# Performance work log

Measured on AMD Instinct MI355X. Metric: run time of the kernel, lower is better.

Reference implementation:

```python
import math
import jax, jax.numpy as jnp
import numpy as np

B, C_IN, H, W = 16, 384, 64, 64
CDIM, K, NSCALES, ITERS = 128, 64, 2, 3

def conv1x1(x, w, b):
    # x: [B,C,H,W], w: [O,C], b: [O]
    return jnp.einsum('bchw,oc->bohw', x, w) + b[None, :, None, None]

def mlp2(x, w1, b1, w2, b2):
    return conv1x1(jax.nn.relu(conv1x1(x, w1, b1)), w2, b2)

def log_optimal_transport(scores, dustbin, iters):
    B_, K_, N_ = scores.shape
    Z = jnp.concatenate([scores, dustbin], axis=1)  # [B,K+1,N]
    log_mu = jnp.full((B_, K_ + 1), -math.log(K_ + 1), dtype=scores.dtype)
    log_nu = jnp.full((B_, N_), -math.log(N_), dtype=scores.dtype)
    u = jnp.zeros_like(log_mu)
    v = jnp.zeros_like(log_nu)
    for _ in range(iters):
        u = log_mu - jax.nn.logsumexp(Z + v[:, None, :], axis=2)
        v = log_nu - jax.nn.logsumexp(Z + u[:, :, None], axis=1)
    return Z + u[:, :, None] + v[:, None, :]

def avg_pool2(x):
    b, c, h, w = x.shape
    return x.reshape(b, c, h // 2, 2, w // 2, 2).mean(axis=(3, 5))

def scale_branch(xs, fw1, fb1, fw2, fb2, sw1, sb1, sw2, sb2, dw1, db1, dw2, db2):
    b = xs.shape[0]
    local_feat = mlp2(xs, fw1, fb1, fw2, fb2).reshape(b, CDIM, -1)   # [B,C,N]
    score = mlp2(xs, sw1, sb1, sw2, sb2).reshape(b, K, -1)           # [B,K,N]
    dustbin = mlp2(xs, dw1, db1, dw2, db2).reshape(b, 1, -1)         # [B,1,N]
    log_p = log_optimal_transport(score, dustbin, ITERS)
    p = jnp.exp(log_p)[:, :-1, :]                                    # drop dustbin row
    p = p / (p.sum(axis=-1, keepdims=True) + 1e-8)
    out = jnp.einsum('bcn,bkn->bck', local_feat, p)                  # [B,C,K]
    out = out / jnp.clip(jnp.linalg.norm(out, axis=1, keepdims=True), 1e-12)
    return out.reshape(b, -1), local_feat

def setup_inputs():
    key = jax.random.key(0)
    ks = jax.random.split(key, 13)
    inp = {'x': jax.random.normal(ks[0], (B, C_IN, H, W), jnp.float32)}
    kidx = 1
    for s in range(NSCALES):
        for name, (o, i) in [('fw1', (512, C_IN)), ('fw2', (CDIM, 512)),
                              ('sw1', (512, C_IN)), ('sw2', (K, 512)),
                              ('dw1', (128, C_IN)), ('dw2', (1, 128))]:
            inp[f'{name}_{s}'] = 0.02 * jax.random.normal(ks[kidx % 13], (o, i), jnp.float32)
            inp[f'{name[0]}b{name[2]}_{s}'] = jnp.zeros((o,), jnp.float32)
            kidx += 1
    return inp

def reference(x,
              fw1_0, fb1_0, fw2_0, fb2_0, sw1_0, sb1_0, sw2_0, sb2_0, dw1_0, db1_0, dw2_0, db2_0,
              fw1_1, fb1_1, fw2_1, fb2_1, sw1_1, sb1_1, sw2_1, sb2_1, dw1_1, db1_1, dw2_1, db2_1):
    params = [
        (fw1_0, fb1_0, fw2_0, fb2_0, sw1_0, sb1_0, sw2_0, sb2_0, dw1_0, db1_0, dw2_0, db2_0),
        (fw1_1, fb1_1, fw2_1, fb2_1, sw1_1, sb1_1, sw2_1, sb2_1, dw1_1, db1_1, dw2_1, db2_1),
    ]
    descs = []
    xs = x
    for s in range(NSCALES):
        if s > 0:
            xs = avg_pool2(xs)
        d, _ = scale_branch(xs, *params[s])
        descs.append(d)
    g = jnp.stack(descs, axis=1).mean(axis=1)
    g = g / jnp.clip(jnp.linalg.norm(g, axis=1, keepdims=True), 1e-12)
    return g
```

## Files before the change

kernel.cpp:

```cpp
#include <hip/hip_runtime.h>
#include <math.h>

typedef __attribute__((ext_vector_type(8))) short short8;
typedef __attribute__((ext_vector_type(4))) float floatx4;

__device__ inline float bf2f(short s) {
    union { unsigned u; float f; } x; x.u = ((unsigned)(unsigned short)s) << 16; return x.f;
}
__device__ inline short f2bf(float f) {
    union { float f; unsigned u; } x; x.f = f;
    unsigned r = x.u + 0x7fff + ((x.u >> 16) & 1);
    return (short)(r >> 16);
}

struct WSet {
    const float *fw1, *fb1, *fw2, *sw1, *sb1, *sw2, *sb2, *dw1, *db1, *dw2, *db2;
};

__device__ inline void wprep_core(const WSet A,
    short* __restrict__ W1f, short* __restrict__ W2af, short* __restrict__ W2bf,
    float* __restrict__ B1p, float* __restrict__ B2bp, int id)
{
    if (id < 491520) {
        int e = id & 7, l = (id >> 3) & 63, g = (id >> 9) & 15, rest = id >> 13;
        int kc = rest % 12, c = rest / 12;
        int m = c * 256 + g * 16 + (l & 15);
        int k = kc * 32 + (l >> 4) * 8 + e;
        float v = 0.f;
        if (m < 512) v = A.fw1[m * 384 + k];
        else if (m < 1024) v = A.sw1[(m - 512) * 384 + k];
        else if (m < 1152) v = A.dw1[(m - 1024) * 384 + k];
        W1f[id] = f2bf(v);
        return;
    }
    id -= 491520;
    if (id < 65536) {
        int e = id & 7, l = (id >> 3) & 63, g = (id >> 9) & 7, ka = id >> 12;
        int r = g * 16 + (l & 15), k = ka * 32 + (l >> 4) * 8 + e;
        W2af[id] = f2bf(A.fw2[r * 512 + k]);
        return;
    }
    id -= 65536;
    if (id < 98304) {
        int e = id & 7, l = (id >> 3) & 63, g = (id >> 9) & 7, kb = id >> 12;
        int r = g * 16 + (l & 15), krel = kb * 32 + (l >> 4) * 8 + e;
        float v = 0.f;
        if (r < 64 && krel < 512) v = A.sw2[r * 512 + krel];
        else if (r == 64 && krel >= 512 && krel < 640) v = A.dw2[krel - 512];
        W2bf[id] = f2bf(v);
        return;
    }
    id -= 98304;
    if (id < 1280) {
        float v = 0.f;
        if (id < 512) v = A.fb1[id];
        else if (id < 1024) v = A.sb1[id - 512];
        else if (id < 1152) v = A.db1[id - 1024];
        B1p[id] = v;
        return;
    }
    id -= 1280;
    if (id < 128) B2bp[id] = id < 64 ? A.sb2[id] : id == 64 ? A.db2[0] : 0.f;
}

__device__ inline void xprep_core(const float* __restrict__ x,
                                  short* __restrict__ xT, short* __restrict__ x1T,
                                  float* xt, int ip, int cg, int b, int t)
{
    #pragma unroll
    for (int u = 0; u < 8; u++) {
        int idx = t + 256 * u;
        int c = idx >> 5, spq = idx & 31;
        float4 v = *(const float4*)&x[(((long)b * 384 + cg * 64 + c) * 64 + ip * 2 + (spq >> 4)) * 64 + (spq & 15) * 4];
        float* d = &xt[c * 129 + spq * 4];
        d[0] = v.x; d[1] = v.y; d[2] = v.z; d[3] = v.w;
    }
    __syncthreads();
    {
        int sp = t >> 1, ch = t & 1;
        short tmp[32];
        #pragma unroll
        for (int cc = 0; cc < 32; cc++) tmp[cc] = f2bf(xt[(ch * 32 + cc) * 129 + sp]);
        short* dst = xT + ((long)b * 4096 + ip * 128 + sp) * 384 + cg * 64 + ch * 32;
        #pragma unroll
        for (int v = 0; v < 4; v++) *(short8*)(dst + v * 8) = *(short8*)(tmp + v * 8);
    }
    {
        int j1 = t >> 3, c8 = t & 7;
        short tmp[8];
        #pragma unroll
        for (int e = 0; e < 8; e++) {
            int c = c8 * 8 + e;
            float v = 0.25f * (xt[c * 129 + j1 * 2]      + xt[c * 129 + j1 * 2 + 1] +
                               xt[c * 129 + 64 + j1 * 2] + xt[c * 129 + 64 + j1 * 2 + 1]);
            tmp[e] = f2bf(v);
        }
        *(short8*)(x1T + ((long)b * 1024 + ip * 32 + j1) * 384 + cg * 64 + c8 * 8) = *(short8*)tmp;
    }
}

__global__ __launch_bounds__(256) void wprep(WSet a0, WSet a1,
    short* __restrict__ W1f, short* __restrict__ W2af, short* __restrict__ W2bf,
    float* __restrict__ B1p, float* __restrict__ B2bp)
{
    const int s = blockIdx.y;
    const WSet A = s ? a1 : a0;
    wprep_core(A, W1f + (size_t)s * 491520, W2af + (size_t)s * 65536,
               W2bf + (size_t)s * 98304, B1p + s * 1280, B2bp + s * 128,
               blockIdx.x * 256 + threadIdx.x);
}

__global__ __launch_bounds__(256) void xprep(const float* __restrict__ x,
                                             short* __restrict__ xT, short* __restrict__ x1T)
{
    __shared__ float xt[64 * 129];
    xprep_core(x, xT, x1T, xt, blockIdx.x, blockIdx.y, blockIdx.z, threadIdx.x);
}

__global__ __launch_bounds__(256) void prep(WSet a0, WSet a1,
    short* __restrict__ W1f, short* __restrict__ W2af, short* __restrict__ W2bf,
    float* __restrict__ B1p, float* __restrict__ B2bp,
    const float* __restrict__ x, short* __restrict__ xT, short* __restrict__ x1T)
{
    __shared__ float xt[64 * 129];
    const int bid = blockIdx.x, t = threadIdx.x;
    if (bid < 5132) {
        const int s = bid >= 2566;
        const WSet A = s ? a1 : a0;
        wprep_core(A, W1f + (size_t)s * 491520, W2af + (size_t)s * 65536,
                   W2bf + (size_t)s * 98304, B1p + s * 1280, B2bp + s * 128,
                   (bid - (s ? 2566 : 0)) * 256 + t);
    } else {
        const int xb = bid - 5132;
        xprep_core(x, xT, x1T, xt, xb & 31, (xb >> 5) % 6, (xb >> 5) / 6, t);
    }
}

__global__ __launch_bounds__(512, 4) void fused_mlp(
    const short* __restrict__ W1f_, const float* __restrict__ B1p_,
    const short* __restrict__ W2af_, const float* __restrict__ fb2_0, const float* __restrict__ fb2_1,
    const short* __restrict__ W2bf_, const float* __restrict__ B2bp_,
    const short* __restrict__ xT, const short* __restrict__ x1T,
    float* __restrict__ feat0, float* __restrict__ feat1,
    short* __restrict__ Eg0, short* __restrict__ Eg1,
    float* __restrict__ pu0, float* __restrict__ pu1)
{
    __shared__ short xs[12 * 2048];
    __shared__ short hs[8 * 2048];
    const int tid = threadIdx.x;
    const int wid = tid >> 6, lane = tid & 63;
    const int l15 = lane & 15, q = lane >> 4;
    const int bx = blockIdx.x, b = blockIdx.y;
    const int sc = bx >= 64;
    const int tile = sc ? bx - 64 : bx;
    const int N = sc ? 1024 : 4096;
    const int n0 = tile * 64;
    const short* XT = sc ? x1T : xT;
    const short* W1f = W1f_ + (size_t)sc * 491520;
    const float* B1p = B1p_ + sc * 1280;
    const short* W2af = W2af_ + (size_t)sc * 65536;
    const short* W2bf = W2bf_ + (size_t)sc * 98304;
    const float* fb2 = sc ? fb2_1 : fb2_0;
    const float* B2bp = B2bp_ + sc * 128;
    float* feat = (sc ? feat1 : feat0) + (long)b * 128 * N;
    short* Eg = (sc ? Eg1 : Eg0) + (long)b * 65 * N;
    float* pu = sc ? pu1 : pu0;
    const int npart = sc ? 16 : 64;

    {
        const int n = tid >> 3;
        const int c0 = (tid & 7) * 6;
        const short* src = XT + ((long)b * N + n0 + n) * 384 + c0 * 8;
        const int jj = n >> 4, nl = n & 15;
        #pragma unroll
        for (int i = 0; i < 6; i++) {
            int c = c0 + i;
            int kc = c >> 2, qq = c & 3;
            *(short8*)(xs + kc * 2048 + jj * 512 + ((qq << 4) | nl) * 8) =
                *(const short8*)(src + i * 8);
        }
    }
    __syncthreads();

    floatx4 acc2[2][4];
    #pragma unroll
    for (int i = 0; i < 2; i++)
        #pragma unroll
        for (int j = 0; j < 4; j++) acc2[i][j] = floatx4{0.f, 0.f, 0.f, 0.f};

    auto phase2 = [&](int pc) {
        if (pc < 2) {
            const short* WA = W2af + (size_t)pc * 32768;
            short8 hb[2][4], wa[2];
            #pragma unroll
            for (int j = 0; j < 4; j++) hb[0][j] = *(short8*)(hs + j * 512 + lane * 8);
            wa[0] = *(const short8*)(WA + wid * 512 + lane * 8);
            #pragma unroll
            for (int kc2 = 0; kc2 < 8; kc2++) {
                short8 bfr[4];
                #pragma unroll
                for (int j = 0; j < 4; j++) bfr[j] = hb[kc2 & 1][j];
                short8 aF = wa[kc2 & 1];
                if (kc2 + 1 < 8) {
                    #pragma unroll
                    for (int j = 0; j < 4; j++)
                        hb[(kc2 + 1) & 1][j] = *(short8*)(hs + (kc2 + 1) * 2048 + j * 512 + lane * 8);
                    wa[(kc2 + 1) & 1] = *(const short8*)(WA + ((kc2 + 1) * 8 + wid) * 512 + lane * 8);
                }
                #pragma unroll
                for (int j = 0; j < 4; j++)
                    acc2[0][j] = __builtin_amdgcn_mfma_f32_16x16x32_bf16(aF, bfr[j], acc2[0][j], 0, 0, 0);
            }
        } else {
            if (wid >= 5) return;
            const short* WB = W2bf + (size_t)(pc - 2) * 32768;
            short8 hb[2][4], we[2];
            #pragma unroll
            for (int j = 0; j < 4; j++) hb[0][j] = *(short8*)(hs + j * 512 + lane * 8);
            we[0] = *(const short8*)(WB + wid * 512 + lane * 8);
            #pragma unroll
            for (int kc2 = 0; kc2 < 8; kc2++) {
                short8 bfr[4];
                #pragma unroll
                for (int j = 0; j < 4; j++) bfr[j] = hb[kc2 & 1][j];
                short8 aE = we[kc2 & 1];
                if (kc2 + 1 < 8) {
                    #pragma unroll
                    for (int j = 0; j < 4; j++)
                        hb[(kc2 + 1) & 1][j] = *(short8*)(hs + (kc2 + 1) * 2048 + j * 512 + lane * 8);
                    we[(kc2 + 1) & 1] = *(const short8*)(WB + ((kc2 + 1) * 8 + wid) * 512 + lane * 8);
                }
                #pragma unroll
                for (int j = 0; j < 4; j++)
                    acc2[1][j] = __builtin_amdgcn_mfma_f32_16x16x32_bf16(aE, bfr[j], acc2[1][j], 0, 0, 0);
            }
        }
    };

    for (int c = 0; c < 5; c++) {
        if (c > 0) phase2(c - 1);
        floatx4 acc1[2][4];
        #pragma unroll
        for (int i = 0; i < 2; i++)
            #pragma unroll
            for (int j = 0; j < 4; j++) acc1[i][j] = floatx4{0.f, 0.f, 0.f, 0.f};
        const short* Wb = W1f + (long)c * 98304;
        short8 abuf[2][2];
        #pragma unroll
        for (int i = 0; i < 2; i++) {
            abuf[0][i] = *(const short8*)(Wb + (wid * 2 + i) * 512 + lane * 8);
            abuf[1][i] = *(const short8*)(Wb + (16 + wid * 2 + i) * 512 + lane * 8);
        }
        #pragma unroll
        for (int kc = 0; kc < 12; kc++) {
            short8 ac[2], bc[4];
            #pragma unroll
            for (int i = 0; i < 2; i++) ac[i] = abuf[kc & 1][i];
            #pragma unroll
            for (int j = 0; j < 4; j++) bc[j] = *(short8*)(xs + kc * 2048 + j * 512 + lane * 8);
            if (kc + 2 < 12) {
                #pragma unroll
                for (int i = 0; i < 2; i++)
                    abuf[kc & 1][i] = *(const short8*)(Wb + ((kc + 2) * 16 + wid * 2 + i) * 512 + lane * 8);
            }
            #pragma unroll
            for (int i = 0; i < 2; i++)
                #pragma unroll
                for (int j = 0; j < 4; j++)
                    acc1[i][j] = __builtin_amdgcn_mfma_f32_16x16x32_bf16(ac[i], bc[j], acc1[i][j], 0, 0, 0);
        }
        __syncthreads();
        #pragma unroll
        for (int i = 0; i < 2; i++) {
            const int qf = i * 2 + (q >> 1);
            const int e0 = 4 * (q & 1);
            const int mrow = c * 256 + wid * 32 + i * 16 + q * 4;
            float bw[4];
            #pragma unroll
            for (int rr = 0; rr < 4; rr++) bw[rr] = B1p[mrow + rr];
            #pragma unroll
            for (int j = 0; j < 4; j++) {
                short pk[4];
                #pragma unroll
                for (int rr = 0; rr < 4; rr++)
                    pk[rr] = f2bf(fmaxf(acc1[i][j][rr] + bw[rr], 0.f));
                *(unsigned long long*)(hs + wid * 2048 + j * 512 + ((qf << 4) | l15) * 8 + e0) =
                    *(unsigned long long*)pk;
            }
        }
        __syncthreads();
    }
    phase2(4);

    {
        const int row0 = wid * 16 + q * 4;
        #pragma unroll
        for (int rr = 0; rr < 4; rr++) {
            float bv = fb2[row0 + rr];
            #pragma unroll
            for (int j = 0; j < 4; j++)
                feat[(long)(row0 + rr) * N + n0 + 16 * j + l15] = acc2[0][j][rr] + bv;
        }
    }
    __syncthreads();
    float* puld = (float*)hs;
    if (wid < 4) {
        #pragma unroll
        for (int rr = 0; rr < 4; rr++) {
            int row = wid * 16 + q * 4 + rr;
            float bv = B2bp[row];
            float s = 0.f;
            #pragma unroll
            for (int j = 0; j < 4; j++) {
                float e = expf(acc2[1][j][rr] + bv);
                Eg[(long)row * N + n0 + 16 * j + l15] = f2bf(e);
                s += e;
            }
            s += __shfl_xor(s, 1); s += __shfl_xor(s, 2);
            s += __shfl_xor(s, 4); s += __shfl_xor(s, 8);
            if (l15 == 0) puld[row] = s;
        }
    } else if (wid == 4) {
        #pragma unroll
        for (int rr = 0; rr < 4; rr++) {
            int row = 64 + q * 4 + rr;
            bool valid = (row == 64);
            float bv = B2bp[64];
            float s = 0.f;
            #pragma unroll
            for (int j = 0; j < 4; j++) {
                float e = expf(acc2[1][j][rr] + bv);
                if (valid) {
                    Eg[(long)64 * N + n0 + 16 * j + l15] = f2bf(e);
                    s += e;
                }
            }
            s += __shfl_xor(s, 1); s += __shfl_xor(s, 2);
            s += __shfl_xor(s, 4); s += __shfl_xor(s, 8);
            if (valid && l15 == 0) puld[64] = s;
        }
    }
    __syncthreads();
    if (tid < 65)
        pu[((long)b * npart + tile) * 65 + tid] = puld[tid];
}

__global__ __launch_bounds__(256) void sk_step(
    const short* __restrict__ Eg0, const short* __restrict__ Eg1,
    const float* __restrict__ pin0, const float* __restrict__ pin1,
    float* __restrict__ pout0, float* __restrict__ pout1, int nin0, int nin1)
{
    __shared__ short Es[65 * 264];
    __shared__ float evs[256];
    __shared__ float eus[65];
    const int t = threadIdx.x;
    const int bx = blockIdx.x, b = blockIdx.y;
    const int sc = bx >= 16;
    const int chunk = sc ? bx - 16 : bx;
    const int N = sc ? 1024 : 4096;
    const float invN = sc ? (1.0f / 1024.0f) : (1.0f / 4096.0f);
    const int n0 = chunk * 256;
    const short* Eb = (sc ? Eg1 : Eg0) + (long)b * 65 * N;
    const float* pin = sc ? pin1 : pin0;
    const int nin = sc ? nin1 : nin0;
    float* pout = sc ? pout1 : pout0;
    const int nout = sc ? 4 : 16;
    if (t < 65) {
        float s = 0.f;
        for (int ch = 0; ch < nin; ch++) s += pin[((long)b * nin + ch) * 65 + t];
        eus[t] = (1.0f / 65.0f) / s;
    }
    for (int it = t; it < 2080; it += 256) {
        int k = it >> 5, n8 = it & 31;
        *(short8*)(Es + k * 264 + n8 * 8) = *(const short8*)(Eb + (long)k * N + n0 + n8 * 8);
    }
    __syncthreads();
    float sv = 0.f;
    #pragma unroll 4
    for (int k = 0; k < 65; k++) sv += bf2f(Es[k * 264 + t]) * eus[k];
    evs[t] = invN / sv;
    __syncthreads();
    const int wid = t >> 6, lane = t & 63;
    for (int k = wid; k < 65; k += 4) {
        const short* er = Es + k * 264 + lane * 4;
        float4 v4 = *(const float4*)&evs[lane * 4];
        float s = bf2f(er[0]) * v4.x + bf2f(er[1]) * v4.y + bf2f(er[2]) * v4.z + bf2f(er[3]) * v4.w;
        #pragma unroll
        for (int off = 32; off >= 1; off >>= 1) s += __shfl_xor(s, off);
        if (lane == 0) pout[((long)b * nout + chunk) * 65 + k] = s;
    }
}

__global__ __launch_bounds__(256) void sk_desc(
    const short* __restrict__ Eg0, const short* __restrict__ Eg1,
    const float* __restrict__ pin0, const float* __restrict__ pin1,
    const float* __restrict__ feat0, const float* __restrict__ feat1,
    float* __restrict__ part0, float* __restrict__ part1, int nin0, int nin1)
{
    __shared__ short Es[65 * 264];
    __shared__ float eus[65];
    __shared__ float evs[256];
    const int t = threadIdx.x;
    const int bx = blockIdx.x, b = blockIdx.y;
    const int sc = bx >= 16;
    const int chunk = sc ? bx - 16 : bx;
    const int N = sc ? 1024 : 4096;
    const float invN = sc ? (1.0f / 1024.0f) : (1.0f / 4096.0f);
    const int nch = sc ? 4 : 16;
    const int n0 = chunk * 256;
    const short* Eb = (sc ? Eg1 : Eg0) + (long)b * 65 * N;
    const float* pin = sc ? pin1 : pin0;
    const int nin = sc ? nin1 : nin0;
    const float* fb = (sc ? feat1 : feat0) + (long)b * 128 * N;
    float* part = sc ? part1 : part0;
    if (t < 65) {
        float s = 0.f;
        for (int ch = 0; ch < nin; ch++) s += pin[((long)b * nin + ch) * 65 + t];
        eus[t] = (1.0f / 65.0f) / s;
    }
    for (int it = t; it < 2080; it += 256) {
        int k = it >> 5, n8 = it & 31;
        *(short8*)(Es + k * 264 + n8 * 8) = *(const short8*)(Eb + (long)k * N + n0 + n8 * 8);
    }
    __syncthreads();
    float sv = 0.f;
    #pragma unroll 4
    for (int k = 0; k < 65; k++) sv += bf2f(Es[k * 264 + t]) * eus[k];
    evs[t] = invN / sv;
    __syncthreads();
    const int wid = t >> 6, lane = t & 63;
    const int l15 = lane & 15, q = lane >> 4;
    float* pb = part + ((long)b * nch + chunk) * 8256;
    for (int k = wid; k < 64; k += 4) {
        const short* er = Es + k * 264 + lane * 4;
        float4 v4 = *(const float4*)&evs[lane * 4];
        float s = bf2f(er[0]) * v4.x + bf2f(er[1]) * v4.y + bf2f(er[2]) * v4.z + bf2f(er[3]) * v4.w;
        #pragma unroll
        for (int off = 32; off >= 1; off >>= 1) s += __shfl_xor(s, off);
        if (lane == 0) pb[8192 + k] = s * eus[k];
    }
    floatx4 acc[2][4];
    #pragma unroll
    for (int mt = 0; mt < 2; mt++)
        #pragma unroll
        for (int nt = 0; nt < 4; nt++) acc[mt][nt] = floatx4{0.f, 0.f, 0.f, 0.f};
    #pragma unroll 2
    for (int ks = 0; ks < 8; ks++) {
        float4 ev0 = *(const float4*)&evs[ks * 32 + q * 8];
        float4 ev1 = *(const float4*)&evs[ks * 32 + q * 8 + 4];
        float evq[8] = {ev0.x, ev0.y, ev0.z, ev0.w, ev1.x, ev1.y, ev1.z, ev1.w};
        short8 ah[2], al[2];
        #pragma unroll
        for (int mt = 0; mt < 2; mt++) {
            const float* fp = fb + (long)(wid * 32 + mt * 16 + l15) * N + n0 + ks * 32 + q * 8;
            float4 v0 = *(const float4*)fp;
            float4 v1 = *(const float4*)(fp + 4);
            float va[8] = {v0.x, v0.y, v0.z, v0.w, v1.x, v1.y, v1.z, v1.w};
            short hh[8], ll[8];
            #pragma unroll
            for (int e = 0; e < 8; e++) {
                float sv2 = va[e] * evq[e];
                short h = f2bf(sv2);
                hh[e] = h;
                ll[e] = f2bf(sv2 - bf2f(h));
            }
            ah[mt] = *(short8*)hh;
            al[mt] = *(short8*)ll;
        }
        #pragma unroll
        for (int nt = 0; nt < 4; nt++) {
            short8 bfr = *(short8*)(Es + (nt * 16 + l15) * 264 + ks * 32 + q * 8);
            #pragma unroll
            for (int mt = 0; mt < 2; mt++) {
                acc[mt][nt] = __builtin_amdgcn_mfma_f32_16x16x32_bf16(al[mt], bfr, acc[mt][nt], 0, 0, 0);
                acc[mt][nt] = __builtin_amdgcn_mfma_f32_16x16x32_bf16(ah[mt], bfr, acc[mt][nt], 0, 0, 0);
            }
        }
    }
    #pragma unroll
    for (int nt = 0; nt < 4; nt++) {
        float euk = eus[nt * 16 + l15];
        #pragma unroll
        for (int mt = 0; mt < 2; mt++)
            #pragma unroll
            for (int rr = 0; rr < 4; rr++)
                pb[(wid * 32 + mt * 16 + q * 4 + rr) * 64 + nt * 16 + l15] = acc[mt][nt][rr] * euk;
    }
}

__global__ __launch_bounds__(256) void dred_final(
    const float* __restrict__ part0, const float* __restrict__ part1,
    float* __restrict__ out, int b0)
{
    __shared__ float d0s[128 * 65];
    __shared__ float d1s[128 * 65];
    __shared__ float rsv[64];
    __shared__ float red[4];
    const int b = blockIdx.x;
    const int t = threadIdx.x;
    const int c = t >> 1, k0 = (t & 1) * 32;

    #pragma unroll
    for (int s = 0; s < 2; s++) {
        const int nch = s ? 4 : 16;
        const float* pb = (s ? part1 : part0) + (long)b * nch * 8256;
        float* ds = s ? d1s : d0s;
        if (t < 64) {
            float rs = 0.f;
            for (int ch = 0; ch < nch; ch++) rs += pb[ch * 8256 + 8192 + t];
            rsv[t] = 1.0f / (rs + 1e-8f);
        }
        __syncthreads();
        float a[32];
        #pragma unroll 8
        for (int j = 0; j < 32; j++) a[j] = 0.f;
        for (int ch = 0; ch < nch; ch++) {
            const float* p = pb + ch * 8256 + c * 64 + k0;
            #pragma unroll 8
            for (int j = 0; j < 32; j++) a[j] += p[j];
        }
        #pragma unroll 8
        for (int j = 0; j < 32; j++) ds[c * 65 + k0 + j] = a[j] * rsv[k0 + j];
        __syncthreads();
        if (t < 64) {
            float sq = 0.f;
            for (int c2 = 0; c2 < 128; c2++) { float v = ds[c2 * 65 + t]; sq += v * v; }
            rsv[t] = 1.0f / fmaxf(sqrtf(sq), 1e-12f);
        }
        __syncthreads();
        #pragma unroll 8
        for (int j = 0; j < 32; j++) ds[c * 65 + k0 + j] *= rsv[k0 + j];
        __syncthreads();
    }
    float s = 0.f;
    for (int i = t; i < 8192; i += 256) {
        int cc = i >> 6, k = i & 63;
        float v = (d0s[cc * 65 + k] + d1s[cc * 65 + k]) * 0.5f;
        s += v * v;
    }
    const int wave = t >> 6, lane = t & 63;
    #pragma unroll
    for (int off = 32; off >= 1; off >>= 1) s += __shfl_xor(s, off);
    if (lane == 0) red[wave] = s;
    __syncthreads();
    float tot = red[0] + red[1] + red[2] + red[3];
    float inv = 1.0f / fmaxf(sqrtf(tot), 1e-12f);
    float* o = out + (long)(b0 + b) * 8192;
    for (int i = t; i < 8192; i += 256) {
        int cc = i >> 6, k = i & 63;
        o[i] = (d0s[cc * 65 + k] + d1s[cc * 65 + k]) * 0.5f * inv;
    }
}

extern "C" void kernel_launch(void* const* d_in, const int* in_sizes, int n_in,
                              void* d_out, int out_size, void* d_ws, size_t ws_size,
                              hipStream_t stream)
{
    (void)in_sizes; (void)n_in; (void)out_size;
    const float* x = (const float*)d_in[0];
    WSet ws2[2];
    const float* fb2p[2];
    for (int s = 0; s < 2; s++) {
        int o = 1 + s * 12;
        ws2[s].fw1 = (const float*)d_in[o + 0];  ws2[s].fb1 = (const float*)d_in[o + 1];
        ws2[s].fw2 = (const float*)d_in[o + 2];  fb2p[s]    = (const float*)d_in[o + 3];
        ws2[s].sw1 = (const float*)d_in[o + 4];  ws2[s].sb1 = (const float*)d_in[o + 5];
        ws2[s].sw2 = (const float*)d_in[o + 6];  ws2[s].sb2 = (const float*)d_in[o + 7];
        ws2[s].dw1 = (const float*)d_in[o + 8];  ws2[s].db1 = (const float*)d_in[o + 9];
        ws2[s].dw2 = (const float*)d_in[o + 10]; ws2[s].db2 = (const float*)d_in[o + 11];
    }

    const size_t fixed = ((size_t)2*491520*2 + 2*65536*2 + 2*98304*2
                        + 2*1280*4 + 2*128*4) + (1 << 16);
    const size_t perb = (size_t)4096*384*2 + (size_t)1024*384*2
                      + (size_t)128*4096*4 + (size_t)128*1024*4
                      + (size_t)65*4096*2 + (size_t)65*1024*2
                      + (size_t)(64+16)*65*4 + (size_t)(16+4)*65*4
                      + (size_t)16*8256*4 + (size_t)4*8256*4 + 8192;
    int CB = 4;
    const int cand[3] = {16, 8, 4};
    for (int ci = 0; ci < 3; ci++)
        if (fixed + (size_t)cand[ci] * perb <= ws_size) { CB = cand[ci]; break; }

    char* p = (char*)d_ws;
    auto alloc = [&](size_t bytes) -> char* {
        char* r = p; p += (bytes + 255) & ~(size_t)255; return r;
    };
    short* W1f   = (short*)alloc((size_t)2 * 491520 * 2);
    short* W2af  = (short*)alloc((size_t)2 * 65536 * 2);
    short* W2bf  = (short*)alloc((size_t)2 * 98304 * 2);
    float* B1p   = (float*)alloc((size_t)2 * 1280 * 4);
    float* B2bp  = (float*)alloc((size_t)2 * 128 * 4);
    short* xT    = (short*)alloc((size_t)CB * 4096 * 384 * 2);
    short* x1T   = (short*)alloc((size_t)CB * 1024 * 384 * 2);
    float* feat0 = (float*)alloc((size_t)CB * 128 * 4096 * 4);
    float* feat1 = (float*)alloc((size_t)CB * 128 * 1024 * 4);
    short* Eg0   = (short*)alloc((size_t)CB * 65 * 4096 * 2);
    short* Eg1   = (short*)alloc((size_t)CB * 65 * 1024 * 2);
    float* puA0  = (float*)alloc((size_t)CB * 64 * 65 * 4);
    float* puA1  = (float*)alloc((size_t)CB * 16 * 65 * 4);
    float* puB0  = (float*)alloc((size_t)CB * 16 * 65 * 4);
    float* puB1  = (float*)alloc((size_t)CB * 4 * 65 * 4);
    float* part0 = (float*)alloc((size_t)CB * 16 * 8256 * 4);
    float* part1 = (float*)alloc((size_t)CB * 4 * 8256 * 4);

    if (CB == 16) {
        prep<<<dim3(8204), 256, 0, stream>>>(ws2[0], ws2[1],
            W1f, W2af, W2bf, B1p, B2bp, x, xT, x1T);
        fused_mlp<<<dim3(80, 16), 512, 0, stream>>>(
            W1f, B1p, W2af, fb2p[0], fb2p[1], W2bf, B2bp,
            xT, x1T, feat0, feat1, Eg0, Eg1, puA0, puA1);
        sk_step<<<dim3(20, 16), 256, 0, stream>>>(Eg0, Eg1, puA0, puA1, puB0, puB1, 64, 16);
        sk_step<<<dim3(20, 16), 256, 0, stream>>>(Eg0, Eg1, puB0, puB1, puA0, puA1, 16, 4);
        sk_desc<<<dim3(20, 16), 256, 0, stream>>>(Eg0, Eg1, puA0, puA1,
                                                  feat0, feat1, part0, part1, 16, 4);
        dred_final<<<dim3(16), 256, 0, stream>>>(part0, part1, (float*)d_out, 0);
    } else {
        wprep<<<dim3(2566, 2), 256, 0, stream>>>(ws2[0], ws2[1], W1f, W2af, W2bf, B1p, B2bp);
        for (int b0 = 0; b0 < 16; b0 += CB) {
            xprep<<<dim3(32, 6, CB), 256, 0, stream>>>(x + (size_t)b0 * 384 * 4096, xT, x1T);
            fused_mlp<<<dim3(80, CB), 512, 0, stream>>>(
                W1f, B1p, W2af, fb2p[0], fb2p[1], W2bf, B2bp,
                xT, x1T, feat0, feat1, Eg0, Eg1, puA0, puA1);
            sk_step<<<dim3(20, CB), 256, 0, stream>>>(Eg0, Eg1, puA0, puA1, puB0, puB1, 64, 16);
            sk_step<<<dim3(20, CB), 256, 0, stream>>>(Eg0, Eg1, puB0, puB1, puA0, puA1, 16, 4);
            sk_desc<<<dim3(20, CB), 256, 0, stream>>>(Eg0, Eg1, puA0, puA1,
                                                      feat0, feat1, part0, part1, 16, 4);
            dred_final<<<dim3(CB), 256, 0, stream>>>(part0, part1, (float*)d_out, b0);
        }
    }
}
```

Baseline: 410.3 us.

## Split fused prep back into separate kernels and widen final reduction to 1024 threads

```diff
diff --git a/kernel.cpp b/kernel.cpp
--- a/kernel.cpp
+++ b/kernel.cpp
@@ -17,10 +17,18 @@
     const float *fw1, *fb1, *fw2, *sw1, *sb1, *sw2, *sb2, *dw1, *db1, *dw2, *db2;
 };
 
-__device__ inline void wprep_core(const WSet A,
+__global__ __launch_bounds__(256) void wprep(WSet a0, WSet a1,
     short* __restrict__ W1f, short* __restrict__ W2af, short* __restrict__ W2bf,
-    float* __restrict__ B1p, float* __restrict__ B2bp, int id)
+    float* __restrict__ B1p, float* __restrict__ B2bp)
 {
+    const int s = blockIdx.y;
+    const WSet A = s ? a1 : a0;
+    W1f  += (size_t)s * 491520;
+    W2af += (size_t)s * 65536;
+    W2bf += (size_t)s * 98304;
+    B1p  += s * 1280;
+    B2bp += s * 128;
+    int id = blockIdx.x * 256 + threadIdx.x;
     if (id < 491520) {
         int e = id & 7, l = (id >> 3) & 63, g = (id >> 9) & 15, rest = id >> 13;
         int kc = rest % 12, c = rest / 12;
@@ -63,10 +71,14 @@
     if (id < 128) B2bp[id] = id < 64 ? A.sb2[id] : id == 64 ? A.db2[0] : 0.f;
 }
 
-__device__ inline void xprep_core(const float* __restrict__ x,
-                                  short* __restrict__ xT, short* __restrict__ x1T,
-                                  float* xt, int ip, int cg, int b, int t)
+__global__ __launch_bounds__(256) void xprep(const float* __restrict__ x,
+                                             short* __restrict__ xT, short* __restrict__ x1T)
 {
+    __shared__ float xt[64 * 129];
+    const int ip = blockIdx.x;
+    const int cg = blockIdx.y;
+    const int b  = blockIdx.z;
+    const int t  = threadIdx.x;
     #pragma unroll
     for (int u = 0; u < 8; u++) {
         int idx = t + 256 * u;
@@ -96,43 +108,6 @@
             tmp[e] = f2bf(v);
         }
         *(short8*)(x1T + ((long)b * 1024 + ip * 32 + j1) * 384 + cg * 64 + c8 * 8) = *(short8*)tmp;
-    }
-}
-
-__global__ __launch_bounds__(256) void wprep(WSet a0, WSet a1,
-    short* __restrict__ W1f, short* __restrict__ W2af, short* __restrict__ W2bf,
-    float* __restrict__ B1p, float* __restrict__ B2bp)
-{
-    const int s = blockIdx.y;
-    const WSet A = s ? a1 : a0;
-    wprep_core(A, W1f + (size_t)s * 491520, W2af + (size_t)s * 65536,
-               W2bf + (size_t)s * 98304, B1p + s * 1280, B2bp + s * 128,
-               blockIdx.x * 256 + threadIdx.x);
-}
-
-__global__ __launch_bounds__(256) void xprep(const float* __restrict__ x,
-                                             short* __restrict__ xT, short* __restrict__ x1T)
-{
-    __shared__ float xt[64 * 129];
-    xprep_core(x, xT, x1T, xt, blockIdx.x, blockIdx.y, blockIdx.z, threadIdx.x);
-}
-
-__global__ __launch_bounds__(256) void prep(WSet a0, WSet a1,
-    short* __restrict__ W1f, short* __restrict__ W2af, short* __restrict__ W2bf,
-    float* __restrict__ B1p, float* __restrict__ B2bp,
-    const float* __restrict__ x, short* __restrict__ xT, short* __restrict__ x1T)
-{
-    __shared__ float xt[64 * 129];
-    const int bid = blockIdx.x, t = threadIdx.x;
-    if (bid < 5132) {
-        const int s = bid >= 2566;
-        const WSet A = s ? a1 : a0;
-        wprep_core(A, W1f + (size_t)s * 491520, W2af + (size_t)s * 65536,
-                   W2bf + (size_t)s * 98304, B1p + s * 1280, B2bp + s * 128,
-                   (bid - (s ? 2566 : 0)) * 256 + t);
-    } else {
-        const int xb = bid - 5132;
-        xprep_core(x, xT, x1T, xt, xb & 31, (xb >> 5) % 6, (xb >> 5) / 6, t);
     }
 }
 
@@ -488,17 +463,20 @@
     }
 }
 
-__global__ __launch_bounds__(256) void dred_final(
+__global__ __launch_bounds__(1024) void dred_final(
     const float* __restrict__ part0, const float* __restrict__ part1,
     float* __restrict__ out, int b0)
 {
     __shared__ float d0s[128 * 65];
     __shared__ float d1s[128 * 65];
+    __shared__ float colp[16][64];
     __shared__ float rsv[64];
-    __shared__ float red[4];
+    __shared__ float red[16];
     const int b = blockIdx.x;
     const int t = threadIdx.x;
-    const int c = t >> 1, k0 = (t & 1) * 32;
+    const int c = t >> 3;
+    const int k0 = (t & 7) * 8;
+    const int wv = t >> 6, l = t & 63;
 
     #pragma unroll
     for (int s = 0; s < 2; s++) {
@@ -511,45 +489,57 @@
             rsv[t] = 1.0f / (rs + 1e-8f);
         }
         __syncthreads();
-        float a[32];
-        #pragma unroll 8
-        for (int j = 0; j < 32; j++) a[j] = 0.f;
+        float a[8];
+        #pragma unroll
+        for (int j = 0; j < 8; j++) a[j] = 0.f;
         for (int ch = 0; ch < nch; ch++) {
             const float* p = pb + ch * 8256 + c * 64 + k0;
-            #pragma unroll 8
-            for (int j = 0; j < 32; j++) a[j] += p[j];
-        }
-        #pragma unroll 8
-        for (int j = 0; j < 32; j++) ds[c * 65 + k0 + j] = a[j] * rsv[k0 + j];
+            #pragma unroll
+            for (int j = 0; j < 8; j++) a[j] += p[j];
+        }
+        #pragma unroll
+        for (int j = 0; j < 8; j++) a[j] *= rsv[k0 + j];
+        float v[8];
+        #pragma unroll
+        for (int j = 0; j < 8; j++) v[j] = a[j] * a[j];
+        #pragma unroll
+        for (int off = 8; off <= 32; off <<= 1)
+            #pragma unroll
+            for (int j = 0; j < 8; j++) v[j] += __shfl_xor(v[j], off);
+        if (l < 8) {
+            #pragma unroll
+            for (int j = 0; j < 8; j++) colp[wv][l * 8 + j] = v[j];
+        }
         __syncthreads();
         if (t < 64) {
             float sq = 0.f;
-            for (int c2 = 0; c2 < 128; c2++) { float v = ds[c2 * 65 + t]; sq += v * v; }
+            #pragma unroll
+            for (int w2 = 0; w2 < 16; w2++) sq += colp[w2][t];
             rsv[t] = 1.0f / fmaxf(sqrtf(sq), 1e-12f);
         }
         __syncthreads();
-        #pragma unroll 8
-        for (int j = 0; j < 32; j++) ds[c * 65 + k0 + j] *= rsv[k0 + j];
+        #pragma unroll
+        for (int j = 0; j < 8; j++) ds[c * 65 + k0 + j] = a[j] * rsv[k0 + j];
         __syncthreads();
     }
-    float s = 0.f;
-    for (int i = t; i < 8192; i += 256) {
-        int cc = i >> 6, k = i & 63;
-        float v = (d0s[cc * 65 + k] + d1s[cc * 65 + k]) * 0.5f;
-        s += v * v;
-    }
-    const int wave = t >> 6, lane = t & 63;
-    #pragma unroll
-    for (int off = 32; off >= 1; off >>= 1) s += __shfl_xor(s, off);
-    if (lane == 0) red[wave] = s;
-    __syncthreads();
-    float tot = red[0] + red[1] + red[2] + red[3];
+    float g[8];
+    float ssum = 0.f;
+    #pragma unroll
+    for (int j = 0; j < 8; j++) {
+        float v2 = (d0s[c * 65 + k0 + j] + d1s[c * 65 + k0 + j]) * 0.5f;
+        g[j] = v2; ssum += v2 * v2;
+    }
+    #pragma unroll
+    for (int off = 32; off >= 1; off >>= 1) ssum += __shfl_xor(ssum, off);
+    if (l == 0) red[wv] = ssum;
+    __syncthreads();
+    float tot = 0.f;
+    #pragma unroll
+    for (int w2 = 0; w2 < 16; w2++) tot += red[w2];
     float inv = 1.0f / fmaxf(sqrtf(tot), 1e-12f);
-    float* o = out + (long)(b0 + b) * 8192;
-    for (int i = t; i < 8192; i += 256) {
-        int cc = i >> 6, k = i & 63;
-        o[i] = (d0s[cc * 65 + k] + d1s[cc * 65 + k]) * 0.5f * inv;
-    }
+    float* o = out + (long)(b0 + b) * 8192 + c * 64 + k0;
+    #pragma unroll
+    for (int j = 0; j < 8; j++) o[j] = g[j] * inv;
 }
 
 extern "C" void kernel_launch(void* const* d_in, const int* in_sizes, int n_in,
@@ -604,29 +594,16 @@
     float* part0 = (float*)alloc((size_t)CB * 16 * 8256 * 4);
     float* part1 = (float*)alloc((size_t)CB * 4 * 8256 * 4);
 
-    if (CB == 16) {
-        prep<<<dim3(8204), 256, 0, stream>>>(ws2[0], ws2[1],
-            W1f, W2af, W2bf, B1p, B2bp, x, xT, x1T);
-        fused_mlp<<<dim3(80, 16), 512, 0, stream>>>(
+    wprep<<<dim3(2566, 2), 256, 0, stream>>>(ws2[0], ws2[1], W1f, W2af, W2bf, B1p, B2bp);
+    for (int b0 = 0; b0 < 16; b0 += CB) {
+        xprep<<<dim3(32, 6, CB), 256, 0, stream>>>(x + (size_t)b0 * 384 * 4096, xT, x1T);
+        fused_mlp<<<dim3(80, CB), 512, 0, stream>>>(
             W1f, B1p, W2af, fb2p[0], fb2p[1], W2bf, B2bp,
             xT, x1T, feat0, feat1, Eg0, Eg1, puA0, puA1);
-        sk_step<<<dim3(20, 16), 256, 0, stream>>>(Eg0, Eg1, puA0, puA1, puB0, puB1, 64, 16);
-        sk_step<<<dim3(20, 16), 256, 0, stream>>>(Eg0, Eg1, puB0, puB1, puA0, puA1, 16, 4);
-        sk_desc<<<dim3(20, 16), 256, 0, stream>>>(Eg0, Eg1, puA0, puA1,
+        sk_step<<<dim3(20, CB), 256, 0, stream>>>(Eg0, Eg1, puA0, puA1, puB0, puB1, 64, 16);
+        sk_step<<<dim3(20, CB), 256, 0, stream>>>(Eg0, Eg1, puB0, puB1, puA0, puA1, 16, 4);
+        sk_desc<<<dim3(20, CB), 256, 0, stream>>>(Eg0, Eg1, puA0, puA1,
                                                   feat0, feat1, part0, part1, 16, 4);
-        dred_final<<<dim3(16), 256, 0, stream>>>(part0, part1, (float*)d_out, 0);
-    } else {
-        wprep<<<dim3(2566, 2), 256, 0, stream>>>(ws2[0], ws2[1], W1f, W2af, W2bf, B1p, B2bp);
-        for (int b0 = 0; b0 < 16; b0 += CB) {
-            xprep<<<dim3(32, 6, CB), 256, 0, stream>>>(x + (size_t)b0 * 384 * 4096, xT, x1T);
-            fused_mlp<<<dim3(80, CB), 512, 0, stream>>>(
-                W1f, B1p, W2af, fb2p[0], fb2p[1], W2bf, B2bp,
-                xT, x1T, feat0, feat1, Eg0, Eg1, puA0, puA1);
-            sk_step<<<dim3(20, CB), 256, 0, stream>>>(Eg0, Eg1, puA0, puA1, puB0, puB1, 64, 16);
-            sk_step<<<dim3(20, CB), 256, 0, stream>>>(Eg0, Eg1, puB0, puB1, puA0, puA1, 16, 4);
-            sk_desc<<<dim3(20, CB), 256, 0, stream>>>(Eg0, Eg1, puA0, puA1,
-                                                      feat0, feat1, part0, part1, 16, 4);
-            dred_final<<<dim3(CB), 256, 0, stream>>>(part0, part1, (float*)d_out, b0);
-        }
-    }
-}
+        dred_final<<<dim3(CB), 1024, 0, stream>>>(part0, part1, (float*)d_out, b0);
+    }
+}
```

After: 398.4 us. -2.9%, faster.
